# Kernel tuning notes

Measured on AMD Instinct MI355X. Metric: run time of the kernel, lower is better.

Reference implementation:

```python
import jax, jax.numpy as jnp
import numpy as np
import math

D_MODEL = 1024
NUM_HEADS = 16
D_HEAD = D_MODEL // NUM_HEADS          # 64
N_FREQ = D_HEAD // 2 + 1               # 33 rfft bins
COMPRESSION_RATIO = 0.5


def setup_inputs() -> dict:
    key = jax.random.key(0)
    k_x, k_qkv, k_out, k_b, k_m = jax.random.split(key, 5)
    B, S = 2, 2048
    x = jax.random.normal(k_x, (B, S, D_MODEL), dtype=jnp.float32)
    # Linear weights stored as [in, out] (torch Linear uses [out, in]; math identical).
    w_qkv = jax.random.normal(k_qkv, (D_MODEL, 3 * D_MODEL), dtype=jnp.float32) / math.sqrt(D_MODEL)
    w_out = jax.random.normal(k_out, (D_MODEL, D_MODEL), dtype=jnp.float32) / math.sqrt(D_MODEL)
    b_out = jax.random.normal(k_b, (D_MODEL,), dtype=jnp.float32) * 0.01
    # Learned per-frequency-bin mask logits of AdaptiveFrequencyMask(d_state=d_head).
    # Initialized around logit(compression_ratio) with small noise.
    init_logit = math.log(COMPRESSION_RATIO / (1.0 - COMPRESSION_RATIO))
    mask_logits = init_logit + 0.1 * jax.random.normal(k_m, (N_FREQ,), dtype=jnp.float32)
    return {"x": x, "w_qkv": w_qkv, "w_out": w_out, "b_out": b_out, "mask_logits": mask_logits}


def _spectral_filter(t, mask):
    # rfft over d_head dim, apply learned soft mask, inverse rfft.  t: [B,H,S,dh]
    tf = jnp.fft.rfft(t, axis=-1)          # [B,H,S,N_FREQ] complex
    tf = tf * mask                          # broadcast real mask over bins
    return jnp.fft.irfft(tf, n=t.shape[-1], axis=-1).astype(t.dtype)


def reference(x, w_qkv, w_out, b_out, mask_logits):
    B, S, D = x.shape
    H, dh = NUM_HEADS, D_HEAD
    qkv = x @ w_qkv                                         # [B,S,3D]
    q, k, v = jnp.split(qkv, 3, axis=-1)
    # [B,S,D] -> [B,H,S,dh]
    to_heads = lambda t: t.reshape(B, S, H, dh).transpose(0, 2, 1, 3)
    q, k, v = to_heads(q), to_heads(k), to_heads(v)
    mask = jax.nn.sigmoid(mask_logits)                      # [N_FREQ]
    q = _spectral_filter(q, mask)
    k = _spectral_filter(k, mask)
    scores = jnp.einsum('bhqd,bhkd->bhqk', q, k) / math.sqrt(dh)
    attn = jax.nn.softmax(scores, axis=-1)                  # dropout p=0 (eval)
    out = jnp.einsum('bhqk,bhkd->bhqd', attn, v)
    out = out.transpose(0, 2, 1, 3).reshape(B, S, D)
    return out @ w_out + b_out
```

## Files before the change

### kernel.cpp

```cpp
#include <hip/hip_runtime.h>

#define S_LEN 2048
#define NH    16
#define DH    64
#define DM    1024
#define NQKV  3072

typedef __attribute__((ext_vector_type(8))) __bf16 bf16x8;
typedef __attribute__((ext_vector_type(4))) float  f32x4;
typedef unsigned short ushort_t;

static __device__ __forceinline__ unsigned short bf16b(float f) {
  return __builtin_bit_cast(unsigned short, (__bf16)f);
}

static __device__ __forceinline__ float exp2v(float x) {
  return __builtin_amdgcn_exp2f(x);
}

static __device__ __forceinline__ bf16x8 pack8(float4 f0, float4 f1) {
  uint4 v;
  v.x = ((unsigned)bf16b(f0.y) << 16) | bf16b(f0.x);
  v.y = ((unsigned)bf16b(f0.w) << 16) | bf16b(f0.z);
  v.z = ((unsigned)bf16b(f1.y) << 16) | bf16b(f1.x);
  v.w = ((unsigned)bf16b(f1.w) << 16) | bf16b(f1.z);
  return __builtin_bit_cast(bf16x8, v);
}

static __device__ __forceinline__ void glds16(const void* g, void* l) {
  __builtin_amdgcn_global_load_lds((const __attribute__((address_space(1))) unsigned int*)g,
                                   (__attribute__((address_space(3))) unsigned int*)l, 16, 0, 0);
}

#define OFF_WT  65536ull
#define OFF_WOT 6356992ull
#define OFF_Q   8454144ull
#define OFF_K   16842752ull
#define OFF_V   25231360ull
#define OFF_AO  33619968ull

__global__ __launch_bounds__(256) void k_prep(const float* __restrict__ wqkv,
                                              const float* __restrict__ wout,
                                              const float* __restrict__ x,
                                              const float* __restrict__ logits,
                                              unsigned short* __restrict__ Wt,
                                              unsigned short* __restrict__ Wot,
                                              unsigned short* __restrict__ xb) {
  __shared__ __align__(16) char sbuf[16640];
  int bid = blockIdx.x;
  int t = threadIdx.x;

  if (bid < 256) {
    float* msk = (float*)sbuf;
    float* Kd  = (float*)(sbuf + 144);
    ushort_t (*Fb)[72] = (ushort_t(*)[72])(sbuf + 416);
    if (t < 33) msk[t] = 1.0f / (1.0f + __expf(-logits[t]));
    __syncthreads();
    if (t < 64) {
      float acc = msk[0];
      #pragma unroll
      for (int f = 1; f < 32; ++f) {
        int r = (f * t) & 63;
        acc += 2.0f * msk[f] * __cosf((float)r * (6.28318530717958647692f / 64.0f));
      }
      acc += msk[32] * ((t & 1) ? -1.0f : 1.0f);
      Kd[t] = acc * (1.0f / 64.0f);
    }
    __syncthreads();
    for (int idx = t; idx < 4096; idx += 256) {
      int j = idx >> 6, i = idx & 63;
      Fb[j][i] = bf16b(Kd[(j - i) & 63]);
    }
    __syncthreads();

    int lane = t & 63, w = t >> 6;
    int m16 = lane & 15, quad = lane >> 4;
    int kx = bid >> 5, yy = bid & 31;
    int which = yy >> 4, h = yy & 15;
    int base = which * 1024 + h * 64;

    bf16x8 af0 = *(const bf16x8*)(&Fb[w * 16 + m16][quad * 8]);
    bf16x8 af1 = *(const bf16x8*)(&Fb[w * 16 + m16][32 + quad * 8]);

    f32x4 acc[8] = {};
    #pragma unroll 2
    for (int n = 0; n < 8; ++n) {
      const float* Wg = wqkv + (size_t)(kx * 128 + n * 16 + m16) * NQKV + base + quad * 8;
      float4 a0 = *(const float4*)(Wg);
      float4 a1 = *(const float4*)(Wg + 4);
      float4 b0 = *(const float4*)(Wg + 32);
      float4 b1 = *(const float4*)(Wg + 36);
      acc[n] = __builtin_amdgcn_mfma_f32_16x16x32_bf16(af0, pack8(a0, a1), acc[n], 0, 0, 0);
      acc[n] = __builtin_amdgcn_mfma_f32_16x16x32_bf16(af1, pack8(b0, b1), acc[n], 0, 0, 0);
    }
    float sc = (which == 0) ? 0.18033688011112042f : 1.0f;
    #pragma unroll
    for (int n = 0; n < 8; ++n) {
      #pragma unroll
      for (int r = 0; r < 4; ++r) {
        int j = w * 16 + quad * 4 + r;
        Wt[(size_t)(base + j) * DM + kx * 128 + n * 16 + m16] = bf16b(acc[n][r] * sc);
      }
    }
  } else if (bid < 768) {
    float (*Ts)[65] = (float(*)[65])sbuf;
    int b1 = bid - 256;
    if (b1 < 256) {
      int kt = b1 & 15, nt = b1 >> 4;
      int cb = 2048 + nt * 64, kbase = kt * 64;
      #pragma unroll
      for (int p = 0; p < 16; ++p) {
        int kk = p * 4 + (t >> 6);
        Ts[kk][t & 63] = wqkv[(size_t)(kbase + kk) * NQKV + cb + (t & 63)];
      }
      __syncthreads();
      #pragma unroll
      for (int p = 0; p < 16; ++p) {
        int nn = p * 4 + (t >> 6);
        Wt[(size_t)(cb + nn) * DM + kbase + (t & 63)] = bf16b(Ts[t & 63][nn]);
      }
    } else {
      int b2 = b1 - 256;
      int kt = b2 & 15, nt = b2 >> 4;
      int cb = nt * 64, kbase = kt * 64;
      #pragma unroll
      for (int p = 0; p < 16; ++p) {
        int kk = p * 4 + (t >> 6);
        Ts[kk][t & 63] = wout[(size_t)(kbase + kk) * DM + cb + (t & 63)];
      }
      __syncthreads();
      #pragma unroll
      for (int p = 0; p < 16; ++p) {
        int nn = p * 4 + (t >> 6);
        Wot[(size_t)(cb + nn) * DM + kbase + (t & 63)] = bf16b(Ts[t & 63][nn]);
      }
    }
  } else {
    size_t i = ((size_t)(bid - 768) * 256 + t) * 8;
    const float4* xp = (const float4*)(x + i);
    float4 a = xp[0], b = xp[1];
    uint4 v;
    v.x = ((unsigned)bf16b(a.y) << 16) | bf16b(a.x);
    v.y = ((unsigned)bf16b(a.w) << 16) | bf16b(a.z);
    v.z = ((unsigned)bf16b(b.y) << 16) | bf16b(b.x);
    v.w = ((unsigned)bf16b(b.w) << 16) | bf16b(b.z);
    *(uint4*)(xb + i) = v;
  }
}

__device__ __forceinline__ void gemm_core_async(const unsigned short* __restrict__ A,
                                                const unsigned short* __restrict__ Bw,
                                                int bm, int bn, unsigned short* smem,
                                                f32x4 (&acc)[4][4]) {
  int t = threadIdx.x, lane = t & 63, w = t >> 6;
  int m16 = lane & 15, quad = lane >> 4;
  int wr = (w >> 1) * 64, wc = (w & 1) * 64;
  int lr = lane >> 3, lc = lane & 7;
  int gc = lc ^ lr;
  int xr = m16 & 7;
  const unsigned short* Agb = A  + (size_t)(bm * 128) * DM + gc * 8;
  const unsigned short* Bgb = Bw + (size_t)(bn * 128) * DM + gc * 8;
  int srow = w * 8 + lr;
  unsigned short* Al = smem + srow * 64 + lc * 8;
  unsigned short* Bl = smem + 8192 + srow * 64 + lc * 8;

  #pragma unroll
  for (int s = 0; s < 4; ++s) {
    #pragma unroll
    for (int p = 0; p < 4; ++p) {
      int row = p * 32 + srow;
      glds16(Agb + (size_t)row * DM + s * 64, Al + s * 16384 + p * 2048);
      glds16(Bgb + (size_t)row * DM + s * 64, Bl + s * 16384 + p * 2048);
    }
  }

  #pragma unroll 1
  for (int wnd = 0; wnd < 8; ++wnd) {
    if (wnd < 7) asm volatile("s_waitcnt vmcnt(16)" ::: "memory");
    else         asm volatile("s_waitcnt vmcnt(0)" ::: "memory");
    __builtin_amdgcn_s_barrier();
    __builtin_amdgcn_sched_barrier(0);
    int sb = (wnd & 1) << 1;
    #pragma unroll
    for (int half = 0; half < 2; ++half) {
      const unsigned short* As = smem + (sb + half) * 16384;
      const unsigned short* Bs = As + 8192;
      #pragma unroll
      for (int kk = 0; kk < 2; ++kk) {
        bf16x8 af[4], bfr[4];
        #pragma unroll
        for (int i = 0; i < 4; ++i)
          af[i] = *(const bf16x8*)(As + (wr + i * 16 + m16) * 64 + ((kk * 4 + quad) ^ xr) * 8);
        #pragma unroll
        for (int j = 0; j < 4; ++j)
          bfr[j] = *(const bf16x8*)(Bs + (wc + j * 16 + m16) * 64 + ((kk * 4 + quad) ^ xr) * 8);
        #pragma unroll
        for (int i = 0; i < 4; ++i)
          #pragma unroll
          for (int j = 0; j < 4; ++j)
            acc[i][j] = __builtin_amdgcn_mfma_f32_16x16x32_bf16(af[i], bfr[j], acc[i][j], 0, 0, 0);
      }
    }
    if (wnd < 6) {
      __builtin_amdgcn_s_barrier();
      int ka = 2 * wnd + 4;
      #pragma unroll
      for (int half = 0; half < 2; ++half) {
        #pragma unroll
        for (int p = 0; p < 4; ++p) {
          int row = p * 32 + srow;
          glds16(Agb + (size_t)row * DM + (ka + half) * 64, Al + (sb + half) * 16384 + p * 2048);
          glds16(Bgb + (size_t)row * DM + (ka + half) * 64, Bl + (sb + half) * 16384 + p * 2048);
        }
      }
    }
  }
  __syncthreads();
}

__global__ __launch_bounds__(256) void k_gemm_qkv(const unsigned short* __restrict__ xb,
                                                  const unsigned short* __restrict__ Bw,
                                                  unsigned short* __restrict__ Qb,
                                                  unsigned short* __restrict__ Kb,
                                                  unsigned short* __restrict__ Vt) {
  __shared__ __align__(16) unsigned short smem[65536];
  f32x4 acc[4][4] = {};
  int bn = blockIdx.x, bm = blockIdx.y;
  gemm_core_async(xb, Bw, bm, bn, smem, acc);

  int t = threadIdx.x, lane = t & 63, w = t >> 6;
  int m16 = lane & 15, quad = lane >> 4;
  int wr = (w >> 1) * 64, wc = (w & 1) * 64;
  int b = bm >> 4, srow = (bm & 15) * 128;
  int which = bn >> 3;
  ushort_t (*Tr)[130] = (ushort_t(*)[130])smem;
  if (which < 2) {
    #pragma unroll
    for (int i = 0; i < 4; ++i)
      #pragma unroll
      for (int j = 0; j < 4; ++j)
        #pragma unroll
        for (int r = 0; r < 4; ++r)
          Tr[wr + i * 16 + quad * 4 + r][wc + j * 16 + m16] = bf16b(acc[i][j][r]);
    __syncthreads();
    int row = t >> 1, half = t & 1;
    int cloc = bn * 128 + half * 64 - which * 1024;
    int h = cloc >> 6;
    unsigned short* dst = (which ? Kb : Qb) +
        ((size_t)(b * 16 + h) * 2048 + srow + row) * 64;
    #pragma unroll
    for (int p = 0; p < 8; ++p)
      *(uint4*)(dst + p * 8) = *(const uint4*)(&Tr[row][half * 64 + p * 8]);
  } else {
    #pragma unroll
    for (int i = 0; i < 4; ++i)
      #pragma unroll
      for (int j = 0; j < 4; ++j)
        #pragma unroll
        for (int r = 0; r < 4; ++r)
          Tr[wc + j * 16 + m16][wr + i * 16 + quad * 4 + r] = bf16b(acc[i][j][r]);
    __syncthreads();
    int dl = t >> 1, half = t & 1;
    int cloc = (bn - 16) * 128 + dl;
    int h = cloc >> 6, d = cloc & 63;
    unsigned short* dst = Vt + ((size_t)(b * 16 + h) * 64 + d) * 2048 + srow + half * 64;
    #pragma unroll
    for (int p = 0; p < 8; ++p)
      *(uint4*)(dst + p * 8) = *(const uint4*)(&Tr[dl][half * 64 + p * 8]);
  }
}

__global__ __launch_bounds__(512, 2) void k_attn(const unsigned short* __restrict__ Qb,
                                                 const unsigned short* __restrict__ Kb,
                                                 const unsigned short* __restrict__ Vt,
                                                 unsigned short* __restrict__ AO) {
  __shared__ __align__(16) unsigned short smem[65536];
  int t = threadIdx.x;
  int w = t >> 6, lane = t & 63;
  int m16 = lane & 15, quad = lane >> 4;
  int bid = blockIdx.x;
  int jj = bid >> 3;
  int bh = ((jj & 3) << 3) + (bid & 7);
  int qbase = (jj >> 2) * 256 + w * 32;

  const unsigned short* QpA = Qb + ((size_t)bh * S_LEN + qbase + m16) * DH + quad * 8;
  const unsigned short* QpB = QpA + 16 * DH;
  bf16x8 aq0A = *(const bf16x8*)(QpA);
  bf16x8 aq1A = *(const bf16x8*)(QpA + 32);
  bf16x8 aq0B = *(const bf16x8*)(QpB);
  bf16x8 aq1B = *(const bf16x8*)(QpB + 32);
  const unsigned short* Kbase = Kb + (size_t)bh * S_LEN * DH;
  const unsigned short* Vbase = Vt + (size_t)bh * DH * S_LEN;

  int xr = m16 & 7;
  unsigned short* Pw = smem + 32768 + w * 4096;

  int trow = t >> 3;
  int tcol = t & 7;
  int gswz = tcol ^ (trow & 7);
  const unsigned short* Kg = Kbase + (size_t)trow * 64 + gswz * 8;
  const unsigned short* Vg = Vbase + (size_t)trow * S_LEN + gswz * 8;
  unsigned short* Kl = smem + trow * 64 + tcol * 8;
  unsigned short* Vl = smem + 16384 + trow * 64 + tcol * 8;

  f32x4 oA[4] = {}, oB[4] = {};
  float lA = 0.f, lB = 0.f;
  f32x4 zero = {0.f, 0.f, 0.f, 0.f};

  #pragma unroll
  for (int tt = 0; tt < 4; ++tt) {
    glds16(Kg + (size_t)tt * 4096, Kl + tt * 4096);
    glds16(Vg + tt * 64,           Vl + tt * 4096);
  }

  #pragma unroll 1
  for (int wnd = 0; wnd < 16; ++wnd) {
    if (wnd < 15) asm volatile("s_waitcnt vmcnt(4)" ::: "memory");
    else          asm volatile("s_waitcnt vmcnt(0)" ::: "memory");
    __builtin_amdgcn_s_barrier();
    __builtin_amdgcn_sched_barrier(0);
    int sb = (wnd & 1) << 1;
    const unsigned short* Ka  = smem + sb * 4096;
    const unsigned short* Kbs = smem + (sb + 1) * 4096;
    const unsigned short* Va  = smem + 16384 + sb * 4096;
    const unsigned short* Vbs = smem + 16384 + (sb + 1) * 4096;
    unsigned short* Pa = Pw;
    unsigned short* Pb = Pw + 2048;

    f32x4 saA[4], saB[4];
    #pragma unroll
    for (int g = 0; g < 4; ++g) {
      int rk = g * 16 + m16;
      bf16x8 kf0 = *(const bf16x8*)(Ka + rk * 64 + ((quad ^ xr) * 8));
      bf16x8 kf1 = *(const bf16x8*)(Ka + rk * 64 + (((4 + quad) ^ xr) * 8));
      saA[g] = __builtin_amdgcn_mfma_f32_16x16x32_bf16(kf0, aq0A, zero, 0, 0, 0);
      saA[g] = __builtin_amdgcn_mfma_f32_16x16x32_bf16(kf1, aq1A, saA[g], 0, 0, 0);
      saB[g] = __builtin_amdgcn_mfma_f32_16x16x32_bf16(kf0, aq0B, zero, 0, 0, 0);
      saB[g] = __builtin_amdgcn_mfma_f32_16x16x32_bf16(kf1, aq1B, saB[g], 0, 0, 0);
    }
    #pragma unroll
    for (int g = 0; g < 4; ++g) {
      int chw = (((2 * g + (quad >> 1)) ^ xr) << 3) + ((quad & 1) << 2);
      float a0 = exp2v(saA[g][0]), a1 = exp2v(saA[g][1]);
      float a2 = exp2v(saA[g][2]), a3 = exp2v(saA[g][3]);
      lA += (a0 + a1) + (a2 + a3);
      uint2 pka;
      pka.x = ((unsigned)bf16b(a1) << 16) | bf16b(a0);
      pka.y = ((unsigned)bf16b(a3) << 16) | bf16b(a2);
      *(uint2*)(Pa + m16 * 64 + chw) = pka;
      float b0 = exp2v(saB[g][0]), b1 = exp2v(saB[g][1]);
      float b2 = exp2v(saB[g][2]), b3 = exp2v(saB[g][3]);
      lB += (b0 + b1) + (b2 + b3);
      uint2 pkb;
      pkb.x = ((unsigned)bf16b(b1) << 16) | bf16b(b0);
      pkb.y = ((unsigned)bf16b(b3) << 16) | bf16b(b2);
      *(uint2*)(Pa + (16 + m16) * 64 + chw) = pkb;
    }
    f32x4 sbA[4], sbB[4];
    #pragma unroll
    for (int g = 0; g < 4; ++g) {
      int rk = g * 16 + m16;
      bf16x8 kf0 = *(const bf16x8*)(Kbs + rk * 64 + ((quad ^ xr) * 8));
      bf16x8 kf1 = *(const bf16x8*)(Kbs + rk * 64 + (((4 + quad) ^ xr) * 8));
      sbA[g] = __builtin_amdgcn_mfma_f32_16x16x32_bf16(kf0, aq0A, zero, 0, 0, 0);
      sbA[g] = __builtin_amdgcn_mfma_f32_16x16x32_bf16(kf1, aq1A, sbA[g], 0, 0, 0);
      sbB[g] = __builtin_amdgcn_mfma_f32_16x16x32_bf16(kf0, aq0B, zero, 0, 0, 0);
      sbB[g] = __builtin_amdgcn_mfma_f32_16x16x32_bf16(kf1, aq1B, sbB[g], 0, 0, 0);
    }
    #pragma unroll
    for (int c = 0; c < 2; ++c) {
      bf16x8 apA = *(const bf16x8*)(Pa + m16 * 64 + (((4 * c + quad) ^ xr) << 3));
      bf16x8 apB = *(const bf16x8*)(Pa + (16 + m16) * 64 + (((4 * c + quad) ^ xr) << 3));
      #pragma unroll
      for (int j = 0; j < 4; ++j) {
        int dv = j * 16 + m16;
        bf16x8 bv = *(const bf16x8*)(Va + dv * 64 + (((c * 4 + quad) ^ xr) * 8));
        oA[j] = __builtin_amdgcn_mfma_f32_16x16x32_bf16(apA, bv, oA[j], 0, 0, 0);
        oB[j] = __builtin_amdgcn_mfma_f32_16x16x32_bf16(apB, bv, oB[j], 0, 0, 0);
      }
    }
    #pragma unroll
    for (int g = 0; g < 4; ++g) {
      int chw = (((2 * g + (quad >> 1)) ^ xr) << 3) + ((quad & 1) << 2);
      float a0 = exp2v(sbA[g][0]), a1 = exp2v(sbA[g][1]);
      float a2 = exp2v(sbA[g][2]), a3 = exp2v(sbA[g][3]);
      lA += (a0 + a1) + (a2 + a3);
      uint2 pka;
      pka.x = ((unsigned)bf16b(a1) << 16) | bf16b(a0);
      pka.y = ((unsigned)bf16b(a3) << 16) | bf16b(a2);
      *(uint2*)(Pb + m16 * 64 + chw) = pka;
      float b0 = exp2v(sbB[g][0]), b1 = exp2v(sbB[g][1]);
      float b2 = exp2v(sbB[g][2]), b3 = exp2v(sbB[g][3]);
      lB += (b0 + b1) + (b2 + b3);
      uint2 pkb;
      pkb.x = ((unsigned)bf16b(b1) << 16) | bf16b(b0);
      pkb.y = ((unsigned)bf16b(b3) << 16) | bf16b(b2);
      *(uint2*)(Pb + (16 + m16) * 64 + chw) = pkb;
    }
    #pragma unroll
    for (int c = 0; c < 2; ++c) {
      bf16x8 apA = *(const bf16x8*)(Pb + m16 * 64 + (((4 * c + quad) ^ xr) << 3));
      bf16x8 apB = *(const bf16x8*)(Pb + (16 + m16) * 64 + (((4 * c + quad) ^ xr) << 3));
      #pragma unroll
      for (int j = 0; j < 4; ++j) {
        int dv = j * 16 + m16;
        bf16x8 bv = *(const bf16x8*)(Vbs + dv * 64 + (((c * 4 + quad) ^ xr) * 8));
        oA[j] = __builtin_amdgcn_mfma_f32_16x16x32_bf16(apA, bv, oA[j], 0, 0, 0);
        oB[j] = __builtin_amdgcn_mfma_f32_16x16x32_bf16(apB, bv, oB[j], 0, 0, 0);
      }
    }
    if (wnd < 14) {
      __builtin_amdgcn_s_barrier();
      int ta = 2 * wnd + 4;
      glds16(Kg + (size_t)ta * 4096,       Kl + sb * 4096);
      glds16(Vg + ta * 64,                 Vl + sb * 4096);
      glds16(Kg + (size_t)(ta + 1) * 4096, Kl + (sb + 1) * 4096);
      glds16(Vg + (ta + 1) * 64,           Vl + (sb + 1) * 4096);
    }
  }

  lA += __shfl_xor(lA, 16); lA += __shfl_xor(lA, 32);
  lB += __shfl_xor(lB, 16); lB += __shfl_xor(lB, 32);
  float ivA = 1.0f / lA;
  float ivB = 1.0f / lB;
  int b = bh >> 4, h = bh & 15;
  #pragma unroll
  for (int r = 0; r < 4; ++r) {
    float vA = __shfl(ivA, quad * 4 + r);
    float vB = __shfl(ivB, quad * 4 + r);
    size_t row0 = (size_t)b * S_LEN + qbase + quad * 4 + r;
    unsigned short* d0 = AO + row0 * DM + h * DH + m16;
    unsigned short* d1 = AO + (row0 + 16) * DM + h * DH + m16;
    #pragma unroll
    for (int j = 0; j < 4; ++j) {
      d0[j * 16] = bf16b(oA[j][r] * vA);
      d1[j * 16] = bf16b(oB[j][r] * vB);
    }
  }
}

__global__ __launch_bounds__(256) void k_gemm_out(const unsigned short* __restrict__ A,
                                                  const unsigned short* __restrict__ Bw,
                                                  const float* __restrict__ bias,
                                                  float* __restrict__ out) {
  __shared__ __align__(16) unsigned short smem[65536];
  f32x4 acc[4][4] = {};
  int bn = blockIdx.x, bm = blockIdx.y;
  gemm_core_async(A, Bw, bm, bn, smem, acc);

  int t = threadIdx.x, lane = t & 63, w = t >> 6;
  int m16 = lane & 15, quad = lane >> 4;
  int wr = (w >> 1) * 64, wc = (w & 1) * 64;
  #pragma unroll
  for (int i = 0; i < 4; ++i) {
    int grow = bm * 128 + wr + i * 16 + quad * 4;
    #pragma unroll
    for (int j = 0; j < 4; ++j) {
      int gc = bn * 128 + wc + j * 16 + m16;
      float bb = bias[gc];
      #pragma unroll
      for (int r = 0; r < 4; ++r)
        out[(size_t)(grow + r) * DM + gc] = acc[i][j][r] + bb;
    }
  }
}

extern "C" void kernel_launch(void* const* d_in, const int* in_sizes, int n_in,
                              void* d_out, int out_size, void* d_ws, size_t ws_size,
                              hipStream_t stream) {
  const float* x    = (const float*)d_in[0];
  const float* wqkv = (const float*)d_in[1];
  const float* wout = (const float*)d_in[2];
  const float* bout = (const float*)d_in[3];
  const float* mlog = (const float*)d_in[4];
  char* ws = (char*)d_ws;
  unsigned short* Wt  = (unsigned short*)(ws + OFF_WT);
  unsigned short* Wot = (unsigned short*)(ws + OFF_WOT);
  unsigned short* Qb  = (unsigned short*)(ws + OFF_Q);
  unsigned short* Kb  = (unsigned short*)(ws + OFF_K);
  unsigned short* Vt  = (unsigned short*)(ws + OFF_V);
  unsigned short* xb  = (unsigned short*)(ws + OFF_AO);
  unsigned short* AO  = (unsigned short*)(ws + OFF_AO);
  float* out = (float*)d_out;

  k_prep<<<dim3(2816), dim3(256), 0, stream>>>(wqkv, wout, x, mlog, Wt, Wot, xb);
  k_gemm_qkv<<<dim3(24, 32), dim3(256), 0, stream>>>(xb, Wt, Qb, Kb, Vt);
  k_attn<<<dim3(256), dim3(512), 0, stream>>>(Qb, Kb, Vt, AO);
  k_gemm_out<<<dim3(8, 32), dim3(256), 0, stream>>>(AO, Wot, bout, out);
}
```

Measured before the change: 187.0 us.

## Enlarge GEMM tiles to 256x256 and 256x128 with 512-thread blocks

Replaces the fixed 128x128 GEMM core with a templated core. The QKV projection now uses 256x256 tiles with 8 waves and the output projection uses 256x128 tiles, both with 512 threads. The pipeline becomes a 2-slot double buffer over 64-wide K steps instead of a 4-slot window. The larger tiles raise arithmetic intensity and cut global traffic per FLOP, but they also shrink the grid (192 and 128 blocks) on a GPU with many CUs and raise register pressure. The QKV epilogue is rewritten to transpose in two chunks through shared memory.

```diff
diff --git a/kernel.cpp b/kernel.cpp
--- a/kernel.cpp
+++ b/kernel.cpp
@@ -148,125 +148,135 @@
   }
 }
 
-__device__ __forceinline__ void gemm_core_async(const unsigned short* __restrict__ A,
-                                                const unsigned short* __restrict__ Bw,
-                                                int bm, int bn, unsigned short* smem,
-                                                f32x4 (&acc)[4][4]) {
+template<int BM, int BN, int WCOLS, int MR, int NR>
+__device__ __forceinline__ void gemm_core2(const unsigned short* __restrict__ A,
+                                           const unsigned short* __restrict__ Bw,
+                                           int bm, int bn, unsigned short* smem,
+                                           f32x4 (&acc)[MR][NR]) {
+  constexpr int SLOT = (BM + BN) * 64;
+  constexpr int PA = BM / 64, PB = BN / 64;
+  constexpr int L = PA + PB;
   int t = threadIdx.x, lane = t & 63, w = t >> 6;
   int m16 = lane & 15, quad = lane >> 4;
-  int wr = (w >> 1) * 64, wc = (w & 1) * 64;
-  int lr = lane >> 3, lc = lane & 7;
-  int gc = lc ^ lr;
+  int wr = (w / WCOLS) * (MR * 16), wc = (w % WCOLS) * (NR * 16);
   int xr = m16 & 7;
-  const unsigned short* Agb = A  + (size_t)(bm * 128) * DM + gc * 8;
-  const unsigned short* Bgb = Bw + (size_t)(bn * 128) * DM + gc * 8;
-  int srow = w * 8 + lr;
-  unsigned short* Al = smem + srow * 64 + lc * 8;
-  unsigned short* Bl = smem + 8192 + srow * 64 + lc * 8;
+  int trow = t >> 3, tcol = t & 7;
+  int gsw = (tcol ^ (trow & 7)) * 8;
+  const unsigned short* Ag = A  + (size_t)(bm * BM + trow) * DM + gsw;
+  const unsigned short* Bg = Bw + (size_t)(bn * BN + trow) * DM + gsw;
+  unsigned short* Al = smem + trow * 64 + tcol * 8;
+  unsigned short* Bl = smem + BM * 64 + trow * 64 + tcol * 8;
 
   #pragma unroll
-  for (int s = 0; s < 4; ++s) {
-    #pragma unroll
-    for (int p = 0; p < 4; ++p) {
-      int row = p * 32 + srow;
-      glds16(Agb + (size_t)row * DM + s * 64, Al + s * 16384 + p * 2048);
-      glds16(Bgb + (size_t)row * DM + s * 64, Bl + s * 16384 + p * 2048);
-    }
+  for (int s = 0; s < 2; ++s) {
+    #pragma unroll
+    for (int p = 0; p < PA; ++p)
+      glds16(Ag + (size_t)p * 64 * DM + s * 64, Al + s * SLOT + p * 4096);
+    #pragma unroll
+    for (int p = 0; p < PB; ++p)
+      glds16(Bg + (size_t)p * 64 * DM + s * 64, Bl + s * SLOT + p * 4096);
   }
 
   #pragma unroll 1
-  for (int wnd = 0; wnd < 8; ++wnd) {
-    if (wnd < 7) asm volatile("s_waitcnt vmcnt(16)" ::: "memory");
+  for (int ks = 0; ks < 16; ++ks) {
+    if (ks < 15) asm volatile("s_waitcnt vmcnt(%0)" :: "n"(L) : "memory");
     else         asm volatile("s_waitcnt vmcnt(0)" ::: "memory");
     __builtin_amdgcn_s_barrier();
     __builtin_amdgcn_sched_barrier(0);
-    int sb = (wnd & 1) << 1;
-    #pragma unroll
-    for (int half = 0; half < 2; ++half) {
-      const unsigned short* As = smem + (sb + half) * 16384;
-      const unsigned short* Bs = As + 8192;
-      #pragma unroll
-      for (int kk = 0; kk < 2; ++kk) {
-        bf16x8 af[4], bfr[4];
+    const unsigned short* As = smem + (ks & 1) * SLOT;
+    const unsigned short* Bs = As + BM * 64;
+    #pragma unroll
+    for (int kk = 0; kk < 2; ++kk) {
+      bf16x8 af[MR], bfr[NR];
+      #pragma unroll
+      for (int i = 0; i < MR; ++i)
+        af[i] = *(const bf16x8*)(As + (wr + i * 16 + m16) * 64 + ((kk * 4 + quad) ^ xr) * 8);
+      #pragma unroll
+      for (int j = 0; j < NR; ++j)
+        bfr[j] = *(const bf16x8*)(Bs + (wc + j * 16 + m16) * 64 + ((kk * 4 + quad) ^ xr) * 8);
+      #pragma unroll
+      for (int i = 0; i < MR; ++i)
         #pragma unroll
-        for (int i = 0; i < 4; ++i)
-          af[i] = *(const bf16x8*)(As + (wr + i * 16 + m16) * 64 + ((kk * 4 + quad) ^ xr) * 8);
+        for (int j = 0; j < NR; ++j)
+          acc[i][j] = __builtin_amdgcn_mfma_f32_16x16x32_bf16(af[i], bfr[j], acc[i][j], 0, 0, 0);
+    }
+    if (ks < 14) {
+      __builtin_amdgcn_s_barrier();
+      __builtin_amdgcn_sched_barrier(0);
+      int kn = ks + 2;
+      #pragma unroll
+      for (int p = 0; p < PA; ++p)
+        glds16(Ag + (size_t)p * 64 * DM + kn * 64, Al + (ks & 1) * SLOT + p * 4096);
+      #pragma unroll
+      for (int p = 0; p < PB; ++p)
+        glds16(Bg + (size_t)p * 64 * DM + kn * 64, Bl + (ks & 1) * SLOT + p * 4096);
+    }
+  }
+  __syncthreads();
+}
+
+__global__ __launch_bounds__(512, 1) void k_gemm_qkv(const unsigned short* __restrict__ xb,
+                                                     const unsigned short* __restrict__ Bw,
+                                                     unsigned short* __restrict__ Qb,
+                                                     unsigned short* __restrict__ Kb,
+                                                     unsigned short* __restrict__ Vt) {
+  __shared__ __align__(16) unsigned short smem[65536];
+  f32x4 acc[8][4] = {};
+  int bn = blockIdx.x, bm = blockIdx.y;
+  gemm_core2<256, 256, 4, 8, 4>(xb, Bw, bm, bn, smem, acc);
+
+  int t = threadIdx.x, lane = t & 63, w = t >> 6;
+  int m16 = lane & 15, quad = lane >> 4;
+  int b = bm >> 3, srow = (bm & 7) * 256;
+  int which = bn >> 2;
+  ushort_t (*Tr)[264] = (ushort_t(*)[264])smem;
+
+  if (which < 2) {
+    unsigned short* dstB = which ? Kb : Qb;
+    int hbase = (bn & 3) * 4;
+    #pragma unroll
+    for (int ch = 0; ch < 2; ++ch) {
+      if ((w >> 2) == ch) {
         #pragma unroll
-        for (int j = 0; j < 4; ++j)
-          bfr[j] = *(const bf16x8*)(Bs + (wc + j * 16 + m16) * 64 + ((kk * 4 + quad) ^ xr) * 8);
-        #pragma unroll
-        for (int i = 0; i < 4; ++i)
+        for (int i = 0; i < 8; ++i)
           #pragma unroll
           for (int j = 0; j < 4; ++j)
-            acc[i][j] = __builtin_amdgcn_mfma_f32_16x16x32_bf16(af[i], bfr[j], acc[i][j], 0, 0, 0);
-      }
-    }
-    if (wnd < 6) {
-      __builtin_amdgcn_s_barrier();
-      int ka = 2 * wnd + 4;
-      #pragma unroll
-      for (int half = 0; half < 2; ++half) {
+            #pragma unroll
+            for (int r = 0; r < 4; ++r)
+              Tr[i * 16 + quad * 4 + r][(w & 3) * 64 + j * 16 + m16] = bf16b(acc[i][j][r]);
+      }
+      __syncthreads();
+      int row = t >> 2, qh = t & 3;
+      unsigned short* dst = dstB +
+          ((size_t)(b * 16 + hbase + qh) * 2048 + srow + ch * 128 + row) * 64;
+      #pragma unroll
+      for (int p = 0; p < 8; ++p)
+        *(uint4*)(dst + p * 8) = *(const uint4*)(&Tr[row][qh * 64 + p * 8]);
+      __syncthreads();
+    }
+  } else {
+    int hb = (bn - 8) * 4;
+    #pragma unroll
+    for (int ch = 0; ch < 2; ++ch) {
+      if (((w >> 1) & 1) == ch) {
         #pragma unroll
-        for (int p = 0; p < 4; ++p) {
-          int row = p * 32 + srow;
-          glds16(Agb + (size_t)row * DM + (ka + half) * 64, Al + (sb + half) * 16384 + p * 2048);
-          glds16(Bgb + (size_t)row * DM + (ka + half) * 64, Bl + (sb + half) * 16384 + p * 2048);
-        }
-      }
-    }
-  }
-  __syncthreads();
-}
-
-__global__ __launch_bounds__(256) void k_gemm_qkv(const unsigned short* __restrict__ xb,
-                                                  const unsigned short* __restrict__ Bw,
-                                                  unsigned short* __restrict__ Qb,
-                                                  unsigned short* __restrict__ Kb,
-                                                  unsigned short* __restrict__ Vt) {
-  __shared__ __align__(16) unsigned short smem[65536];
-  f32x4 acc[4][4] = {};
-  int bn = blockIdx.x, bm = blockIdx.y;
-  gemm_core_async(xb, Bw, bm, bn, smem, acc);
-
-  int t = threadIdx.x, lane = t & 63, w = t >> 6;
-  int m16 = lane & 15, quad = lane >> 4;
-  int wr = (w >> 1) * 64, wc = (w & 1) * 64;
-  int b = bm >> 4, srow = (bm & 15) * 128;
-  int which = bn >> 3;
-  ushort_t (*Tr)[130] = (ushort_t(*)[130])smem;
-  if (which < 2) {
-    #pragma unroll
-    for (int i = 0; i < 4; ++i)
-      #pragma unroll
-      for (int j = 0; j < 4; ++j)
-        #pragma unroll
-        for (int r = 0; r < 4; ++r)
-          Tr[wr + i * 16 + quad * 4 + r][wc + j * 16 + m16] = bf16b(acc[i][j][r]);
-    __syncthreads();
-    int row = t >> 1, half = t & 1;
-    int cloc = bn * 128 + half * 64 - which * 1024;
-    int h = cloc >> 6;
-    unsigned short* dst = (which ? Kb : Qb) +
-        ((size_t)(b * 16 + h) * 2048 + srow + row) * 64;
-    #pragma unroll
-    for (int p = 0; p < 8; ++p)
-      *(uint4*)(dst + p * 8) = *(const uint4*)(&Tr[row][half * 64 + p * 8]);
-  } else {
-    #pragma unroll
-    for (int i = 0; i < 4; ++i)
-      #pragma unroll
-      for (int j = 0; j < 4; ++j)
-        #pragma unroll
-        for (int r = 0; r < 4; ++r)
-          Tr[wc + j * 16 + m16][wr + i * 16 + quad * 4 + r] = bf16b(acc[i][j][r]);
-    __syncthreads();
-    int dl = t >> 1, half = t & 1;
-    int cloc = (bn - 16) * 128 + dl;
-    int h = cloc >> 6, d = cloc & 63;
-    unsigned short* dst = Vt + ((size_t)(b * 16 + h) * 64 + d) * 2048 + srow + half * 64;
-    #pragma unroll
-    for (int p = 0; p < 8; ++p)
-      *(uint4*)(dst + p * 8) = *(const uint4*)(&Tr[dl][half * 64 + p * 8]);
+        for (int i = 0; i < 8; ++i)
+          #pragma unroll
+          for (int j = 0; j < 4; ++j)
+            #pragma unroll
+            for (int r = 0; r < 4; ++r)
+              Tr[(w & 1) * 64 + j * 16 + m16][(w >> 2) * 128 + i * 16 + quad * 4 + r] =
+                  bf16b(acc[i][j][r]);
+      }
+      __syncthreads();
+      int c = t >> 2, qh = t & 3;
+      int h = hb + ch * 2 + (c >> 6), d = c & 63;
+      unsigned short* dst = Vt + ((size_t)(b * 16 + h) * 64 + d) * 2048 + srow;
+      #pragma unroll
+      for (int p = 0; p < 8; ++p)
+        *(uint4*)(dst + qh * 64 + p * 8) = *(const uint4*)(&Tr[c][qh * 64 + p * 8]);
+      __syncthreads();
+    }
   }
 }
 
@@ -439,21 +449,21 @@
   }
 }
 
-__global__ __launch_bounds__(256) void k_gemm_out(const unsigned short* __restrict__ A,
-                                                  const unsigned short* __restrict__ Bw,
-                                                  const float* __restrict__ bias,
-                                                  float* __restrict__ out) {
-  __shared__ __align__(16) unsigned short smem[65536];
+__global__ __launch_bounds__(512, 1) void k_gemm_out(const unsigned short* __restrict__ A,
+                                                     const unsigned short* __restrict__ Bw,
+                                                     const float* __restrict__ bias,
+                                                     float* __restrict__ out) {
+  __shared__ __align__(16) unsigned short smem[49152];
   f32x4 acc[4][4] = {};
   int bn = blockIdx.x, bm = blockIdx.y;
-  gemm_core_async(A, Bw, bm, bn, smem, acc);
+  gemm_core2<256, 128, 2, 4, 4>(A, Bw, bm, bn, smem, acc);
 
   int t = threadIdx.x, lane = t & 63, w = t >> 6;
   int m16 = lane & 15, quad = lane >> 4;
   int wr = (w >> 1) * 64, wc = (w & 1) * 64;
   #pragma unroll
   for (int i = 0; i < 4; ++i) {
-    int grow = bm * 128 + wr + i * 16 + quad * 4;
+    int grow = bm * 256 + wr + i * 16 + quad * 4;
     #pragma unroll
     for (int j = 0; j < 4; ++j) {
       int gc = bn * 128 + wc + j * 16 + m16;
@@ -484,7 +494,7 @@
   float* out = (float*)d_out;
 
   k_prep<<<dim3(2816), dim3(256), 0, stream>>>(wqkv, wout, x, mlog, Wt, Wot, xb);
-  k_gemm_qkv<<<dim3(24, 32), dim3(256), 0, stream>>>(xb, Wt, Qb, Kb, Vt);
+  k_gemm_qkv<<<dim3(12, 16), dim3(512), 0, stream>>>(xb, Wt, Qb, Kb, Vt);
   k_attn<<<dim3(256), dim3(512), 0, stream>>>(Qb, Kb, Vt, AO);
-  k_gemm_out<<<dim3(8, 32), dim3(256), 0, stream>>>(AO, Wot, bout, out);
-}
+  k_gemm_out<<<dim3(8, 16), dim3(512), 0, stream>>>(AO, Wot, bout, out);
+}
```

Result: no change. 189.9 us (+1.6%).
